# Kernel tuning notes

Hardware: AMD Instinct MI355X
Metric: run time of the kernel (lower is better)

## Reference

```python
import jax, jax.numpy as jnp
import numpy as np

N, E, B, F_IN, C, K = 200000, 3200000, 128, 128, 10, 30
D_CAT = 97  # 32+32+32+1 concatenated GCN outputs


def setup_inputs() -> dict:
    key = jax.random.key(0)
    ks = jax.random.split(key, 12)
    s = 0.1
    return {
        "x": jax.random.normal(ks[0], (N, F_IN), jnp.float32),
        "edge_index": jax.random.randint(ks[1], (2, E), 0, N, jnp.int32),
        "batch": jnp.sort(jax.random.randint(ks[2], (N,), 0, B, jnp.int32)),
        "W1": jax.random.normal(ks[3], (F_IN, 32), jnp.float32) * s,
        "b1": jnp.zeros((32,), jnp.float32),
        "W2": jax.random.normal(ks[4], (32, 32), jnp.float32) * s,
        "b2": jnp.zeros((32,), jnp.float32),
        "W3": jax.random.normal(ks[5], (32, 32), jnp.float32) * s,
        "b3": jnp.zeros((32,), jnp.float32),
        "W4": jax.random.normal(ks[6], (32, 1), jnp.float32) * s,
        "b4": jnp.zeros((1,), jnp.float32),
        "conv5_w": jax.random.normal(ks[7], (16, 1, 97), jnp.float32) * s,
        "conv5_b": jnp.zeros((16,), jnp.float32),
        "conv6_w": jax.random.normal(ks[8], (32, 16, 5), jnp.float32) * s,
        "conv6_b": jnp.zeros((32,), jnp.float32),
        "fc1_w": jax.random.normal(ks[9], (352, 128), jnp.float32) * s,
        "fc1_b": jnp.zeros((128,), jnp.float32),
        "fc2_w": jax.random.normal(ks[10], (128, C), jnp.float32) * s,
        "fc2_b": jnp.zeros((C,), jnp.float32),
    }


def _gcn(x, W, b, src, dst, enorm, self_norm):
    # PyG GCNConv: h = xW; out = sum_j norm_ij * h_j (incl. self loop) + b
    h = x @ W
    agg = jax.ops.segment_sum(h[src] * enorm[:, None], dst, num_segments=h.shape[0])
    return agg + h * self_norm[:, None] + b


def _conv1d(x, w, b, stride):
    y = jax.lax.conv_general_dilated(x, w, (stride,), 'VALID',
                                     dimension_numbers=('NCH', 'OIH', 'NCH'))
    return y + b[None, :, None]


def reference(x, edge_index, batch, W1, b1, W2, b2, W3, b3, W4, b4,
              conv5_w, conv5_b, conv6_w, conv6_b, fc1_w, fc1_b, fc2_w, fc2_b):
    src, dst = edge_index[0], edge_index[1]
    # remove_self_loops (zero edge weight) then GCN adds self loop of weight 1
    w = (src != dst).astype(x.dtype)
    deg = jax.ops.segment_sum(w, dst, num_segments=N) + 1.0
    dinv = jax.lax.rsqrt(deg)
    enorm = w * dinv[src] * dinv[dst]   # per-edge sym norm
    self_norm = 1.0 / deg               # self-loop norm = dinv[i]^2

    x1 = jnp.tanh(_gcn(x, W1, b1, src, dst, enorm, self_norm))
    x2 = jnp.tanh(_gcn(x1, W2, b2, src, dst, enorm, self_norm))
    x3 = jnp.tanh(_gcn(x2, W3, b3, src, dst, enorm, self_norm))
    x4 = jnp.tanh(_gcn(x3, W4, b4, src, dst, enorm, self_norm))
    xc = jnp.concatenate([x1, x2, x3, x4], axis=-1)  # [N, 97]

    # SortAggregation(k=30): per-graph top-k nodes by last channel (descending)
    keyf = xc[:, -1]
    graph_ids = jnp.arange(B, dtype=batch.dtype)
    scores = jnp.where(batch[None, :] == graph_ids[:, None], keyf[None, :],
                       jnp.float32(-jnp.inf))         # [B, N]
    topv, topi = jax.lax.top_k(scores, K)              # [B, K]
    feats = xc[topi]                                   # [B, K, 97]
    feats = jnp.where(jnp.isfinite(topv)[..., None], feats, 0.0)  # pad rows -> 0
    z = feats.reshape(B, 1, K * D_CAT)                 # [B, 1, 2910]

    z = jax.nn.relu(_conv1d(z, conv5_w, conv5_b, 97))  # [B, 16, 30]
    z = jax.lax.reduce_window(z, -jnp.inf, jax.lax.max,
                              (1, 1, 2), (1, 1, 2), 'VALID')  # [B, 16, 15]
    z = jax.nn.relu(_conv1d(z, conv6_w, conv6_b, 1))   # [B, 32, 11]
    z = z.reshape(B, -1)                               # [B, 352]
    h = jax.nn.relu(z @ fc1_w + fc1_b)                 # dropout = identity (eval)
    return jax.nn.log_softmax(h @ fc2_w + fc2_b, axis=-1)
```

## Files before the change

### kernel.cpp

```cpp
#include <hip/hip_runtime.h>
#include <math.h>

#define TPB 256
#define TOPK 30
#define NGRAPH 128
#define TKCAP 4096
#define BSHIFT 11
#define NBMAX 128
#define FSHIFT 8
#define NFMAX 800
#define FCAP 4608


__global__ void bhist(const int* __restrict__ src, const int* __restrict__ dst,
                      int* __restrict__ btot, int E) {
    __shared__ int bcnt[NBMAX];
    int t = threadIdx.x;
    int base = blockIdx.x * 2048;
    int lim = E - base; if (lim > 2048) lim = 2048;
    for (int i = t; i < NBMAX; i += 256) bcnt[i] = 0;
    __syncthreads();
    for (int i = t; i < lim; i += 256) {
        int s = src[base + i], d = dst[base + i];
        if (s != d) atomicAdd(&bcnt[d >> BSHIFT], 1);
    }
    __syncthreads();
    for (int i = t; i < NBMAX; i += 256)
        if (bcnt[i] > 0) atomicAdd(&btot[i], bcnt[i]);
}

__global__ void bucket_scan(const int* __restrict__ btot, int* __restrict__ bbase,
                            int nbuckets) {
    __shared__ int ls[NBMAX];
    int t = threadIdx.x;
    int v = (t < nbuckets) ? btot[t] : 0;
    ls[t] = v;
    __syncthreads();
    for (int o = 1; o < NBMAX; o <<= 1) {
        int x = 0;
        if (t >= o) x = ls[t - o];
        __syncthreads();
        ls[t] += x;
        __syncthreads();
    }
    if (t < nbuckets) bbase[t] = ls[t] - v;
}

__global__ void bin_edges(const int* __restrict__ src, const int* __restrict__ dst,
                          const int* __restrict__ bbase_g, int* __restrict__ gcur,
                          int2* __restrict__ scratch, int E) {
    __shared__ int2 eds[2048];
    __shared__ int bcnt[NBMAX], bbase[NBMAX], boff[NBMAX];
    int t = threadIdx.x;
    int base = blockIdx.x * 2048;
    int lim = E - base; if (lim > 2048) lim = 2048;
    for (int i = t; i < NBMAX; i += 256) { bcnt[i] = 0; boff[i] = 0; }
    __syncthreads();
    for (int i = t; i < lim; i += 256) {
        int s = src[base + i], d = dst[base + i];
        if (s == d) d = -1;
        eds[i] = make_int2(s, d);
        if (d >= 0) atomicAdd(&bcnt[d >> BSHIFT], 1);
    }
    __syncthreads();
    for (int i = t; i < NBMAX; i += 256) {
        if (bcnt[i] > 0)
            bbase[i] = bbase_g[i] + atomicAdd(&gcur[i], bcnt[i]);
    }
    __syncthreads();
    for (int i = t; i < lim; i += 256) {
        int2 ed = eds[i];
        if (ed.y >= 0) {
            int b = ed.y >> BSHIFT;
            int pos = bbase[b] + atomicAdd(&boff[b], 1);
            scratch[pos] = ed;
        }
    }
}

__global__ void bucket_count(const int2* __restrict__ scratch,
                             const int* __restrict__ bbase, const int* __restrict__ btot,
                             int* __restrict__ cnt, float* __restrict__ dinv,
                             float* __restrict__ snorm, int N) {
    __shared__ int hist[1 << BSHIFT];
    int b = blockIdx.x, t = threadIdx.x;
    int nlo = b << BSHIFT;
    int nn = N - nlo; if (nn > (1 << BSHIFT)) nn = 1 << BSHIFT;
    for (int i = t; i < (1 << BSHIFT); i += 256) hist[i] = 0;
    __syncthreads();
    int lo = bbase[b], hi = lo + btot[b];
    for (int e = lo + t; e < hi; e += 256)
        atomicAdd(&hist[scratch[e].y - nlo], 1);
    __syncthreads();
    for (int i = t; i < nn; i += 256) {
        int c = hist[i];
        cnt[nlo + i] = c;
        float deg = (float)c + 1.0f;
        dinv[nlo + i] = 1.0f / sqrtf(deg);
        snorm[nlo + i] = 1.0f / deg;
    }
}

__global__ void scan1(const int* __restrict__ cnt, int* __restrict__ outp,
                      int* __restrict__ bsum, int n) {
    __shared__ int ls[256];
    int t = threadIdx.x;
    int base = blockIdx.x * 1024;
    int v[4], ex[4];
    int run = 0;
    #pragma unroll
    for (int j = 0; j < 4; ++j) {
        int i = base + t * 4 + j;
        v[j] = (i < n) ? cnt[i] : 0;
        ex[j] = run;
        run += v[j];
    }
    ls[t] = run;
    __syncthreads();
    for (int o2 = 1; o2 < 256; o2 <<= 1) {
        int xv = 0;
        if (t >= o2) xv = ls[t - o2];
        __syncthreads();
        ls[t] += xv;
        __syncthreads();
    }
    int tbase = ls[t] - run;
    #pragma unroll
    for (int j = 0; j < 4; ++j) {
        int i = base + t * 4 + j;
        if (i < n) outp[i] = tbase + ex[j];
    }
    if (t == 255) bsum[blockIdx.x] = ls[255];
}

__global__ void scan2(int* __restrict__ bsum, int nb) {
    __shared__ int ls[256];
    int t = threadIdx.x;
    int v = (t < nb) ? bsum[t] : 0;
    ls[t] = v;
    __syncthreads();
    for (int o2 = 1; o2 < 256; o2 <<= 1) {
        int xv = 0;
        if (t >= o2) xv = ls[t - o2];
        __syncthreads();
        ls[t] += xv;
        __syncthreads();
    }
    if (t < nb) bsum[t] = ls[t] - v;
    if (t == 255) bsum[nb] = ls[255];
}

__global__ void scan3(int* __restrict__ rowptr, const int* __restrict__ bsum, int n, int nb) {
    int i = blockIdx.x * blockDim.x + threadIdx.x;
    if (i < n) rowptr[i] += bsum[i >> 10];
    if (i == 0) rowptr[n] = bsum[nb];
}

__global__ void bin2(const int2* __restrict__ scratch, const int* __restrict__ rowptr,
                     int* __restrict__ fcur, int2* __restrict__ scratch2, int N, int E) {
    __shared__ int fcnt[NFMAX], fbase[NFMAX], foff[NFMAX];
    int t = threadIdx.x;
    int En = rowptr[N];
    int base = blockIdx.x * 8192;
    if (base >= En) return;
    int lim = En - base; if (lim > 8192) lim = 8192;
    for (int i = t; i < NFMAX; i += 256) { fcnt[i] = 0; foff[i] = 0; }
    __syncthreads();
    for (int i = t; i < lim; i += 256) {
        int d = scratch[base + i].y;
        atomicAdd(&fcnt[d >> FSHIFT], 1);
    }
    __syncthreads();
    for (int fi = t; fi < NFMAX; fi += 256) {
        if (fcnt[fi] > 0)
            fbase[fi] = rowptr[fi << FSHIFT] + atomicAdd(&fcur[fi], fcnt[fi]);
    }
    __syncthreads();
    for (int i = t; i < lim; i += 256) {
        int2 ed = scratch[base + i];
        int fi = ed.y >> FSHIFT;
        int pos = fbase[fi] + atomicAdd(&foff[fi], 1);
        scratch2[pos] = ed;
    }
}

__global__ __launch_bounds__(256) void scatter_sort(const int2* __restrict__ scratch2,
                                                    const int* __restrict__ rowptr,
                                                    const float* __restrict__ dinv,
                                                    int2* __restrict__ eprec, int N) {
    __shared__ int srcA[FCAP], dstA[FCAP], inv[FCAP];
    __shared__ int hist[1 << FSHIFT];
    __shared__ int hcur[1 << FSHIFT];
    int f = blockIdx.x, t = threadIdx.x;
    int nlo = f << FSHIFT;
    int nhi = nlo + (1 << FSHIFT); if (nhi > N) nhi = N;
    int lo = rowptr[nlo], hi = rowptr[nhi];
    int span = hi - lo;
    for (int i = t; i < (1 << FSHIFT); i += 256) hist[i] = 0;
    __syncthreads();
    if (span <= FCAP) {
        for (int i = t; i < span; i += 256) {
            int2 ed = scratch2[lo + i];
            srcA[i] = ed.x; dstA[i] = ed.y;
            atomicAdd(&hist[ed.y - nlo], 1);
        }
        __syncthreads();
        int v = hist[t];
        hcur[t] = v;
        __syncthreads();
        for (int o = 1; o < 256; o <<= 1) {
            int x = (t >= o) ? hcur[t - o] : 0;
            __syncthreads();
            hcur[t] += x;
            __syncthreads();
        }
        int excl = hcur[t] - v;
        __syncthreads();
        hcur[t] = excl;
        __syncthreads();
        for (int i = t; i < span; i += 256) {
            int slot = atomicAdd(&hcur[dstA[i] - nlo], 1);
            inv[slot] = i;
        }
        __syncthreads();
        for (int p = t; p < span; p += 256) {
            int i = inv[p];
            int s = srcA[i], d = dstA[i];
            eprec[lo + p] = make_int2(s, __float_as_int(dinv[s] * dinv[d]));
        }
    } else {
        for (int e = lo + t; e < hi; e += 256) {
            int2 ed = scratch2[e];
            int d = ed.y;
            int p = rowptr[d] + atomicAdd(&hist[d - nlo], 1);
            eprec[p] = make_int2(ed.x, __float_as_int(dinv[ed.x] * dinv[d]));
        }
    }
}


__global__ void mm_128_32(const float* __restrict__ X, const float* __restrict__ W,
                          float* __restrict__ H, int n) {
    __shared__ float Ws[128 * 32];
    __shared__ float xs[32 * 128];
    int t = threadIdx.x;
    int rbase = blockIdx.x * 32;
    #pragma unroll
    for (int j = 0; j < 4; ++j) {
        int idx = t + 256 * j;
        *(float4*)(Ws + idx * 4) = *(const float4*)(W + idx * 4);
        int row = rbase + (idx >> 5);
        float4 v = make_float4(0.f, 0.f, 0.f, 0.f);
        if (row < n) v = *(const float4*)(X + (long)rbase * 128 + idx * 4);
        *(float4*)(xs + idx * 4) = v;
    }
    __syncthreads();
    int c4 = (t & 7) * 4, r = t >> 3;
    int row = rbase + r;
    if (row >= n) return;
    float ac0 = 0.f, ac1 = 0.f, ac2 = 0.f, ac3 = 0.f;
    #pragma unroll 8
    for (int k0 = 0; k0 < 128; k0 += 4) {
        float4 xv = *(const float4*)(xs + r * 128 + k0);
        #pragma unroll
        for (int j = 0; j < 4; ++j) {
            float xj = (j == 0) ? xv.x : (j == 1) ? xv.y : (j == 2) ? xv.z : xv.w;
            float4 wv = *(const float4*)(Ws + (k0 + j) * 32 + c4);
            ac0 += xj * wv.x; ac1 += xj * wv.y; ac2 += xj * wv.z; ac3 += xj * wv.w;
        }
    }
    *(float4*)(H + (long)row * 32 + c4) = make_float4(ac0, ac1, ac2, ac3);
}

__global__ void mm_32_32(const float* __restrict__ X, const float* __restrict__ W,
                         float* __restrict__ H, int n) {
    __shared__ float Ws[32 * 32];
    __shared__ float xs[32 * 32];
    int t = threadIdx.x;
    int rbase = blockIdx.x * 32;
    {
        *(float4*)(Ws + t * 4) = *(const float4*)(W + t * 4);
        int row = rbase + (t >> 3);
        float4 v = make_float4(0.f, 0.f, 0.f, 0.f);
        if (row < n) v = *(const float4*)(X + (long)rbase * 32 + t * 4);
        *(float4*)(xs + t * 4) = v;
    }
    __syncthreads();
    int c4 = (t & 7) * 4, r = t >> 3;
    int row = rbase + r;
    if (row >= n) return;
    float ac0 = 0.f, ac1 = 0.f, ac2 = 0.f, ac3 = 0.f;
    #pragma unroll
    for (int k0 = 0; k0 < 32; k0 += 4) {
        float4 xv = *(const float4*)(xs + r * 32 + k0);
        #pragma unroll
        for (int j = 0; j < 4; ++j) {
            float xj = (j == 0) ? xv.x : (j == 1) ? xv.y : (j == 2) ? xv.z : xv.w;
            float4 wv = *(const float4*)(Ws + (k0 + j) * 32 + c4);
            ac0 += xj * wv.x; ac1 += xj * wv.y; ac2 += xj * wv.z; ac3 += xj * wv.w;
        }
    }
    *(float4*)(H + (long)row * 32 + c4) = make_float4(ac0, ac1, ac2, ac3);
}

__global__ void mm_32_1(const float* __restrict__ X, const float* __restrict__ W,
                        float* __restrict__ H4, int n) {
    int gid = blockIdx.x * blockDim.x + threadIdx.x;
    int node = gid >> 3, l = gid & 7;
    if (node >= n) return;
    float4 v = *(const float4*)(X + (long)node * 32 + l * 4);
    float s = v.x * W[l * 4] + v.y * W[l * 4 + 1] + v.z * W[l * 4 + 2] + v.w * W[l * 4 + 3];
    s += __shfl_xor(s, 1, 64);
    s += __shfl_xor(s, 2, 64);
    s += __shfl_xor(s, 4, 64);
    if (l == 0) H4[node] = s;
}


__global__ void agg32(const float* __restrict__ H, const int2* __restrict__ eprec,
                      const int* __restrict__ rowptr,
                      const float* __restrict__ snorm, const float* __restrict__ bias,
                      float* __restrict__ OUT, int n) {
    int gid = blockIdx.x * blockDim.x + threadIdx.x;
    int node = gid >> 3, l = gid & 7;
    if (node >= n) return;
    int beg = rowptr[node], end = rowptr[node + 1];
    float ax = 0.f, ay = 0.f, az = 0.f, aw = 0.f;
    int e0 = beg;
    for (; e0 + 8 <= end; e0 += 8) {
        int2 ed = eprec[e0 + l];
        int ss[8]; float ww[8];
        #pragma unroll
        for (int j = 0; j < 8; ++j) {
            ss[j] = __shfl(ed.x, j, 8);
            ww[j] = __shfl(__int_as_float(ed.y), j, 8);
        }
        float4 hv[8];
        #pragma unroll
        for (int j = 0; j < 8; ++j)
            hv[j] = *(const float4*)(H + (long)ss[j] * 32 + l * 4);
        #pragma unroll
        for (int j = 0; j < 8; ++j) {
            ax += hv[j].x * ww[j]; ay += hv[j].y * ww[j];
            az += hv[j].z * ww[j]; aw += hv[j].w * ww[j];
        }
    }
    if (e0 < end) {
        int m = end - e0;
        int2 ed = (l < m) ? eprec[e0 + l] : make_int2(0, 0);
        for (int j = 0; j < m; ++j) {
            int s = __shfl(ed.x, j, 8);
            float w = __shfl(__int_as_float(ed.y), j, 8);
            float4 hv = *(const float4*)(H + (long)s * 32 + l * 4);
            ax += hv.x * w; ay += hv.y * w; az += hv.z * w; aw += hv.w * w;
        }
    }
    float sn = snorm[node];
    float4 hv = *(const float4*)(H + (long)node * 32 + l * 4);
    float4 bv = *(const float4*)(bias + l * 4);
    float4 o;
    o.x = tanhf(ax + hv.x * sn + bv.x);
    o.y = tanhf(ay + hv.y * sn + bv.y);
    o.z = tanhf(az + hv.z * sn + bv.z);
    o.w = tanhf(aw + hv.w * sn + bv.w);
    *(float4*)(OUT + (long)node * 32 + l * 4) = o;
}

__global__ void agg1(const float* __restrict__ H4, const int2* __restrict__ eprec,
                     const int* __restrict__ rowptr,
                     const float* __restrict__ snorm, const float* __restrict__ b4,
                     float* __restrict__ X4, int n) {
    int node = blockIdx.x * blockDim.x + threadIdx.x;
    if (node >= n) return;
    int beg = rowptr[node], end = rowptr[node + 1];
    float acc = 0.f;
    for (int e = beg; e < end; ++e) {
        int2 ed = eprec[e];
        acc += H4[ed.x] * __int_as_float(ed.y);
    }
    X4[node] = tanhf(acc + H4[node] * snorm[node] + b4[0]);
}


__global__ void graph_start(const int* __restrict__ batch, int* __restrict__ gstart,
                            int n, int B) {
    int i = blockIdx.x * blockDim.x + threadIdx.x;
    if (i >= n) return;
    int b = batch[i];
    int bp = (i == 0) ? -1 : batch[i - 1];
    for (int g = bp + 1; g <= b; ++g) gstart[g] = i;
    if (i == n - 1) {
        for (int g = b + 1; g <= B; ++g) gstart[g] = n;
    }
}

__global__ __launch_bounds__(64) void topk_kernel(const float* __restrict__ keyf,
                                                  const int* __restrict__ gstart,
                                                  int* __restrict__ topi) {
    int g = blockIdx.x;
    int t = threadIdx.x;
    __shared__ float vals[TKCAP];
    __shared__ int selg[TOPK];
    int beg = gstart[g], end = gstart[g + 1];
    int range = end - beg;

    if (range <= 2048) {
        float rv[32];
        #pragma unroll
        for (int j = 0; j < 32; ++j) {
            int i = t + (j << 6);
            rv[j] = (i < range) ? keyf[beg + i] : -INFINITY;
        }
        for (int k = 0; k < TOPK; ++k) {
            float best = -INFINITY;
            int bj = -1;
            #pragma unroll
            for (int j = 0; j < 32; ++j)
                if (rv[j] > best) { best = rv[j]; bj = j; }
            int bi = (bj < 0) ? 0x7fffffff : (bj << 6) + t;
            #pragma unroll
            for (int off = 1; off < 64; off <<= 1) {
                float ov = __shfl_xor(best, off, 64);
                int oi = __shfl_xor(bi, off, 64);
                if (ov > best || (ov == best && oi < bi)) { best = ov; bi = oi; }
            }
            if (t == 0)
                topi[g * TOPK + k] = (bi == 0x7fffffff) ? -1 : beg + bi;
            if (bi != 0x7fffffff && (bi & 63) == t) {
                int wj = bi >> 6;
                #pragma unroll
                for (int j = 0; j < 32; ++j)
                    if (j == wj) rv[j] = -INFINITY;
            }
        }
        return;
    }

    int lim = range < TKCAP ? range : TKCAP;
    for (int i = t; i < lim; i += 64) vals[i] = keyf[beg + i];
    __syncthreads();
    for (int k = 0; k < TOPK; ++k) {
        float best = -INFINITY;
        int bi = 0x7fffffff;
        for (int i = t; i < lim; i += 64) {
            float v = vals[i];
            if (v > best) { best = v; bi = i; }
        }
        for (int i = TKCAP + t; i < range; i += 64) {
            int gi = beg + i;
            bool taken = false;
            for (int j = 0; j < k; ++j)
                if (selg[j] == gi) { taken = true; break; }
            if (taken) continue;
            float v = keyf[gi];
            if (v > best || (v == best && i < bi)) { best = v; bi = i; }
        }
        #pragma unroll
        for (int off = 1; off < 64; off <<= 1) {
            float ov = __shfl_xor(best, off, 64);
            int oi = __shfl_xor(bi, off, 64);
            if (ov > best || (ov == best && oi < bi)) { best = ov; bi = oi; }
        }
        if (t == 0) {
            int gl = (bi == 0x7fffffff) ? -1 : beg + bi;
            selg[k] = gl;
            topi[g * TOPK + k] = gl;
            if (bi != 0x7fffffff && bi < TKCAP) vals[bi] = -INFINITY;
        }
        __syncthreads();
    }
}


__global__ void head_kernel(const float* __restrict__ x1, const float* __restrict__ x2,
                            const float* __restrict__ x3, const float* __restrict__ x4,
                            const int* __restrict__ topi,
                            const float* __restrict__ w5, const float* __restrict__ b5,
                            const float* __restrict__ w6, const float* __restrict__ b6,
                            const float* __restrict__ fw1, const float* __restrict__ fb1,
                            const float* __restrict__ fw2, const float* __restrict__ fb2,
                            float* __restrict__ out) {
    int b = blockIdx.x;
    int t = threadIdx.x;
    __shared__ float feats[TOPK][97];
    __shared__ float c5[16][30];
    __shared__ float p6[16][15];
    __shared__ float z[352];
    __shared__ float hh[128];
    __shared__ float oo[10];

    for (int idx = t; idx < TOPK * 97; idx += 256) {
        int k = idx / 97, j = idx % 97;
        int node = topi[b * TOPK + k];
        float v = 0.f;
        if (node >= 0) {
            if (j < 32) v = x1[(long)node * 32 + j];
            else if (j < 64) v = x2[(long)node * 32 + (j - 32)];
            else if (j < 96) v = x3[(long)node * 32 + (j - 64)];
            else v = x4[node];
        }
        feats[k][j] = v;
    }
    __syncthreads();

    for (int idx = t; idx < 16 * 30; idx += 256) {
        int oc = idx / 30, k = idx % 30;
        float acc = b5[oc];
        for (int j = 0; j < 97; ++j) acc += w5[oc * 97 + j] * feats[k][j];
        c5[oc][k] = fmaxf(acc, 0.f);
    }
    __syncthreads();

    for (int idx = t; idx < 16 * 15; idx += 256) {
        int oc = idx / 15, k = idx % 15;
        p6[oc][k] = fmaxf(c5[oc][2 * k], c5[oc][2 * k + 1]);
    }
    __syncthreads();

    for (int idx = t; idx < 32 * 11; idx += 256) {
        int oc = idx / 11, tt = idx % 11;
        float acc = b6[oc];
        for (int ic = 0; ic < 16; ++ic)
            for (int j = 0; j < 5; ++j)
                acc += w6[(oc * 16 + ic) * 5 + j] * p6[ic][tt + j];
        z[idx] = fmaxf(acc, 0.f);
    }
    __syncthreads();

    if (t < 128) {
        float acc = fb1[t];
        for (int i = 0; i < 352; ++i) acc += z[i] * fw1[i * 128 + t];
        hh[t] = fmaxf(acc, 0.f);
    }
    __syncthreads();

    if (t < 10) {
        float acc = fb2[t];
        for (int j = 0; j < 128; ++j) acc += hh[j] * fw2[j * 10 + t];
        oo[t] = acc;
    }
    __syncthreads();

    if (t < 10) {
        float m = -INFINITY;
        for (int c = 0; c < 10; ++c) m = fmaxf(m, oo[c]);
        float s = 0.f;
        for (int c = 0; c < 10; ++c) s += expf(oo[c] - m);
        out[b * 10 + t] = oo[t] - m - logf(s);
    }
}


extern "C" void kernel_launch(void* const* d_in, const int* in_sizes, int n_in,
                              void* d_out, int out_size, void* d_ws, size_t ws_size,
                              hipStream_t stream) {
    const float* x     = (const float*)d_in[0];
    const int*   ei    = (const int*)d_in[1];
    const int*   batch = (const int*)d_in[2];
    const float* W1 = (const float*)d_in[3];
    const float* b1 = (const float*)d_in[4];
    const float* W2 = (const float*)d_in[5];
    const float* b2 = (const float*)d_in[6];
    const float* W3 = (const float*)d_in[7];
    const float* b3 = (const float*)d_in[8];
    const float* W4 = (const float*)d_in[9];
    const float* b4 = (const float*)d_in[10];
    const float* w5 = (const float*)d_in[11];
    const float* b5 = (const float*)d_in[12];
    const float* w6 = (const float*)d_in[13];
    const float* b6 = (const float*)d_in[14];
    const float* fw1 = (const float*)d_in[15];
    const float* fb1 = (const float*)d_in[16];
    const float* fw2 = (const float*)d_in[17];
    const float* fb2 = (const float*)d_in[18];

    const int N = in_sizes[0] / 128;
    const int E = in_sizes[1] / 2;
    const int* src = ei;
    const int* dst = ei + E;

    char* w = (char*)d_ws;
    size_t off = 0;
    auto alloc = [&](size_t bytes) -> void* {
        void* p = w + off;
        off = (off + bytes + 255) & ~(size_t)255;
        return p;
    };

    int*   cnt    = (int*)alloc((size_t)N * 4);
    int*   rowptr = (int*)alloc((size_t)(N + 1) * 4);
    int*   bsum   = (int*)alloc(4096 * 4);
    int*   gcur   = (int*)alloc(NBMAX * 4);
    int*   btot   = (int*)alloc(NBMAX * 4);
    int*   bbase  = (int*)alloc(NBMAX * 4);
    int*   fcur   = (int*)alloc(NFMAX * 4);
    float* dinv   = (float*)alloc((size_t)N * 4);
    float* snorm  = (float*)alloc((size_t)N * 4);
    int2*  eprec  = (int2*)alloc((size_t)E * 8);
    float* hbuf   = (float*)alloc((size_t)N * 32 * 4);
    float* x1     = (float*)alloc((size_t)N * 32 * 4);
    float* x2     = (float*)alloc((size_t)N * 32 * 4);
    float* x3     = (float*)alloc((size_t)N * 32 * 4);
    float* h4     = (float*)alloc((size_t)N * 4);
    float* x4     = (float*)alloc((size_t)N * 4);
    int*   gstart = (int*)alloc((size_t)(NGRAPH + 1) * 4);
    int*   topi   = (int*)alloc((size_t)NGRAPH * TOPK * 4);

    int2* scratch  = (int2*)hbuf;
    int2* scratch2 = (int2*)x1;

    hipMemsetAsync(gcur, 0, NBMAX * 4, stream);
    hipMemsetAsync(btot, 0, NBMAX * 4, stream);
    hipMemsetAsync(fcur, 0, NFMAX * 4, stream);

    const int NB = (N + (1 << BSHIFT) - 1) >> BSHIFT;
    const int NF = (N + (1 << FSHIFT) - 1) >> FSHIFT;
    const int EB = (E + 2047) / 2048;

    bhist<<<EB, TPB, 0, stream>>>(src, dst, btot, E);
    bucket_scan<<<1, NBMAX, 0, stream>>>(btot, bbase, NB);
    bin_edges<<<EB, TPB, 0, stream>>>(src, dst, bbase, gcur, scratch, E);
    bucket_count<<<NB, TPB, 0, stream>>>(scratch, bbase, btot, cnt, dinv, snorm, N);

    int nb = (N + 1023) / 1024;
    scan1<<<nb, 256, 0, stream>>>(cnt, rowptr, bsum, N);
    scan2<<<1, 256, 0, stream>>>(bsum, nb);
    scan3<<<(N + TPB - 1) / TPB, TPB, 0, stream>>>(rowptr, bsum, N, nb);

    bin2<<<(E + 8191) / 8192, TPB, 0, stream>>>(scratch, rowptr, fcur, scratch2, N, E);
    scatter_sort<<<NF, 256, 0, stream>>>(scratch2, rowptr, dinv, eprec, N);

    mm_128_32<<<(N + 31) / 32, 256, 0, stream>>>(x, W1, hbuf, N);
    agg32<<<((size_t)N * 8 + TPB - 1) / TPB, TPB, 0, stream>>>(hbuf, eprec, rowptr,
                                                               snorm, b1, x1, N);
    mm_32_32<<<(N + 31) / 32, 256, 0, stream>>>(x1, W2, hbuf, N);
    agg32<<<((size_t)N * 8 + TPB - 1) / TPB, TPB, 0, stream>>>(hbuf, eprec, rowptr,
                                                               snorm, b2, x2, N);
    mm_32_32<<<(N + 31) / 32, 256, 0, stream>>>(x2, W3, hbuf, N);
    agg32<<<((size_t)N * 8 + TPB - 1) / TPB, TPB, 0, stream>>>(hbuf, eprec, rowptr,
                                                               snorm, b3, x3, N);
    mm_32_1<<<((size_t)N * 8 + TPB - 1) / TPB, TPB, 0, stream>>>(x3, W4, h4, N);
    agg1<<<(N + TPB - 1) / TPB, TPB, 0, stream>>>(h4, eprec, rowptr, snorm, b4, x4, N);

    graph_start<<<(N + TPB - 1) / TPB, TPB, 0, stream>>>(batch, gstart, N, NGRAPH);
    topk_kernel<<<NGRAPH, 64, 0, stream>>>(x4, gstart, topi);
    head_kernel<<<NGRAPH, 256, 0, stream>>>(x1, x2, x3, x4, topi, w5, b5, w6, b6,
                                            fw1, fb1, fw2, fb2, (float*)d_out);
}
```

Before: 563.0 us.

## Fold CSR scan into bucket_count, drop bin2 pass, fuse top-k with head

Each coarse bucket now computes its own per-node exclusive scan offset from the bucket base, which replaces the three global scan kernels. The second binning pass goes away: each fine block scans its whole coarse bucket and keeps only edges whose destination falls in its range. Graph boundaries are found by binary search over batch, and top-k selection is fused into the head kernel. This cuts kernel launches and one full edge copy, at the cost of each coarse bucket being read eight times in scatter_sort.

```diff
diff --git a/kernel.cpp b/kernel.cpp
--- a/kernel.cpp
+++ b/kernel.cpp
@@ -8,7 +8,6 @@
 #define BSHIFT 11
 #define NBMAX 128
 #define FSHIFT 8
-#define NFMAX 800
 #define FCAP 4608
 
 
@@ -80,9 +79,10 @@
 
 __global__ void bucket_count(const int2* __restrict__ scratch,
                              const int* __restrict__ bbase, const int* __restrict__ btot,
-                             int* __restrict__ cnt, float* __restrict__ dinv,
-                             float* __restrict__ snorm, int N) {
+                             int* __restrict__ rowptr, float* __restrict__ dinv,
+                             float* __restrict__ snorm, int N, int NB) {
     __shared__ int hist[1 << BSHIFT];
+    __shared__ int ls2[256];
     int b = blockIdx.x, t = threadIdx.x;
     int nlo = b << BSHIFT;
     int nn = N - nlo; if (nn > (1 << BSHIFT)) nn = 1 << BSHIFT;
@@ -92,117 +92,60 @@
     for (int e = lo + t; e < hi; e += 256)
         atomicAdd(&hist[scratch[e].y - nlo], 1);
     __syncthreads();
-    for (int i = t; i < nn; i += 256) {
-        int c = hist[i];
-        cnt[nlo + i] = c;
-        float deg = (float)c + 1.0f;
-        dinv[nlo + i] = 1.0f / sqrtf(deg);
-        snorm[nlo + i] = 1.0f / deg;
-    }
-}
-
-__global__ void scan1(const int* __restrict__ cnt, int* __restrict__ outp,
-                      int* __restrict__ bsum, int n) {
-    __shared__ int ls[256];
-    int t = threadIdx.x;
-    int base = blockIdx.x * 1024;
-    int v[4], ex[4];
-    int run = 0;
+    int loc[8]; int run = 0;
     #pragma unroll
-    for (int j = 0; j < 4; ++j) {
-        int i = base + t * 4 + j;
-        v[j] = (i < n) ? cnt[i] : 0;
-        ex[j] = run;
-        run += v[j];
-    }
-    ls[t] = run;
-    __syncthreads();
-    for (int o2 = 1; o2 < 256; o2 <<= 1) {
-        int xv = 0;
-        if (t >= o2) xv = ls[t - o2];
-        __syncthreads();
-        ls[t] += xv;
-        __syncthreads();
-    }
-    int tbase = ls[t] - run;
+    for (int j = 0; j < 8; ++j) { loc[j] = run; run += hist[t * 8 + j]; }
+    ls2[t] = run;
+    __syncthreads();
+    for (int o = 1; o < 256; o <<= 1) {
+        int x = (t >= o) ? ls2[t - o] : 0;
+        __syncthreads();
+        ls2[t] += x;
+        __syncthreads();
+    }
+    int base = bbase[b] + ls2[t] - run;
     #pragma unroll
-    for (int j = 0; j < 4; ++j) {
-        int i = base + t * 4 + j;
-        if (i < n) outp[i] = tbase + ex[j];
-    }
-    if (t == 255) bsum[blockIdx.x] = ls[255];
-}
-
-__global__ void scan2(int* __restrict__ bsum, int nb) {
-    __shared__ int ls[256];
-    int t = threadIdx.x;
-    int v = (t < nb) ? bsum[t] : 0;
-    ls[t] = v;
-    __syncthreads();
-    for (int o2 = 1; o2 < 256; o2 <<= 1) {
-        int xv = 0;
-        if (t >= o2) xv = ls[t - o2];
-        __syncthreads();
-        ls[t] += xv;
-        __syncthreads();
-    }
-    if (t < nb) bsum[t] = ls[t] - v;
-    if (t == 255) bsum[nb] = ls[255];
-}
-
-__global__ void scan3(int* __restrict__ rowptr, const int* __restrict__ bsum, int n, int nb) {
-    int i = blockIdx.x * blockDim.x + threadIdx.x;
-    if (i < n) rowptr[i] += bsum[i >> 10];
-    if (i == 0) rowptr[n] = bsum[nb];
-}
-
-__global__ void bin2(const int2* __restrict__ scratch, const int* __restrict__ rowptr,
-                     int* __restrict__ fcur, int2* __restrict__ scratch2, int N, int E) {
-    __shared__ int fcnt[NFMAX], fbase[NFMAX], foff[NFMAX];
-    int t = threadIdx.x;
-    int En = rowptr[N];
-    int base = blockIdx.x * 8192;
-    if (base >= En) return;
-    int lim = En - base; if (lim > 8192) lim = 8192;
-    for (int i = t; i < NFMAX; i += 256) { fcnt[i] = 0; foff[i] = 0; }
-    __syncthreads();
-    for (int i = t; i < lim; i += 256) {
-        int d = scratch[base + i].y;
-        atomicAdd(&fcnt[d >> FSHIFT], 1);
-    }
-    __syncthreads();
-    for (int fi = t; fi < NFMAX; fi += 256) {
-        if (fcnt[fi] > 0)
-            fbase[fi] = rowptr[fi << FSHIFT] + atomicAdd(&fcur[fi], fcnt[fi]);
-    }
-    __syncthreads();
-    for (int i = t; i < lim; i += 256) {
-        int2 ed = scratch[base + i];
-        int fi = ed.y >> FSHIFT;
-        int pos = fbase[fi] + atomicAdd(&foff[fi], 1);
-        scratch2[pos] = ed;
-    }
-}
-
-__global__ __launch_bounds__(256) void scatter_sort(const int2* __restrict__ scratch2,
+    for (int j = 0; j < 8; ++j) {
+        int i = t * 8 + j;
+        if (i < nn) {
+            rowptr[nlo + i] = base + loc[j];
+            int c = hist[i];
+            float deg = (float)c + 1.0f;
+            dinv[nlo + i] = 1.0f / sqrtf(deg);
+            snorm[nlo + i] = 1.0f / deg;
+        }
+    }
+    if (b == NB - 1 && t == 0) rowptr[N] = bbase[b] + btot[b];
+}
+
+__global__ __launch_bounds__(256) void scatter_sort(const int2* __restrict__ scratch,
+                                                    const int* __restrict__ bbase,
+                                                    const int* __restrict__ btot,
                                                     const int* __restrict__ rowptr,
                                                     const float* __restrict__ dinv,
                                                     int2* __restrict__ eprec, int N) {
     __shared__ int srcA[FCAP], dstA[FCAP], inv[FCAP];
     __shared__ int hist[1 << FSHIFT];
     __shared__ int hcur[1 << FSHIFT];
+    __shared__ int kcnt;
     int f = blockIdx.x, t = threadIdx.x;
     int nlo = f << FSHIFT;
     int nhi = nlo + (1 << FSHIFT); if (nhi > N) nhi = N;
     int lo = rowptr[nlo], hi = rowptr[nhi];
     int span = hi - lo;
+    int cb = f >> (BSHIFT - FSHIFT);
+    int clo = bbase[cb], chi = clo + btot[cb];
     for (int i = t; i < (1 << FSHIFT); i += 256) hist[i] = 0;
+    if (t == 0) kcnt = 0;
     __syncthreads();
     if (span <= FCAP) {
-        for (int i = t; i < span; i += 256) {
-            int2 ed = scratch2[lo + i];
-            srcA[i] = ed.x; dstA[i] = ed.y;
-            atomicAdd(&hist[ed.y - nlo], 1);
+        for (int e = clo + t; e < chi; e += 256) {
+            int2 ed = scratch[e];
+            if ((ed.y >> FSHIFT) == f) {
+                int p = atomicAdd(&kcnt, 1);
+                srcA[p] = ed.x; dstA[p] = ed.y;
+                atomicAdd(&hist[ed.y - nlo], 1);
+            }
         }
         __syncthreads();
         int v = hist[t];
@@ -229,11 +172,13 @@
             eprec[lo + p] = make_int2(s, __float_as_int(dinv[s] * dinv[d]));
         }
     } else {
-        for (int e = lo + t; e < hi; e += 256) {
-            int2 ed = scratch2[e];
-            int d = ed.y;
-            int p = rowptr[d] + atomicAdd(&hist[d - nlo], 1);
-            eprec[p] = make_int2(ed.x, __float_as_int(dinv[ed.x] * dinv[d]));
+        for (int e = clo + t; e < chi; e += 256) {
+            int2 ed = scratch[e];
+            if ((ed.y >> FSHIFT) == f) {
+                int d = ed.y;
+                int p = rowptr[d] + atomicAdd(&hist[d - nlo], 1);
+                eprec[p] = make_int2(ed.x, __float_as_int(dinv[ed.x] * dinv[d]));
+            }
         }
     }
 }
@@ -382,106 +327,23 @@
 }
 
 
-__global__ void graph_start(const int* __restrict__ batch, int* __restrict__ gstart,
-                            int n, int B) {
-    int i = blockIdx.x * blockDim.x + threadIdx.x;
-    if (i >= n) return;
-    int b = batch[i];
-    int bp = (i == 0) ? -1 : batch[i - 1];
-    for (int g = bp + 1; g <= b; ++g) gstart[g] = i;
-    if (i == n - 1) {
-        for (int g = b + 1; g <= B; ++g) gstart[g] = n;
-    }
-}
-
-__global__ __launch_bounds__(64) void topk_kernel(const float* __restrict__ keyf,
-                                                  const int* __restrict__ gstart,
-                                                  int* __restrict__ topi) {
+__global__ __launch_bounds__(256) void topk_head(
+        const float* __restrict__ x1, const float* __restrict__ x2,
+        const float* __restrict__ x3, const float* __restrict__ x4,
+        const int* __restrict__ batch, int Nn,
+        const float* __restrict__ w5, const float* __restrict__ b5,
+        const float* __restrict__ w6, const float* __restrict__ b6,
+        const float* __restrict__ fw1, const float* __restrict__ fb1,
+        const float* __restrict__ fw2, const float* __restrict__ fb2,
+        float* __restrict__ out) {
     int g = blockIdx.x;
     int t = threadIdx.x;
+    __shared__ int topi_l[TOPK];
+    __shared__ int selg[TOPK];
+    __shared__ int begend[2];
     __shared__ float vals[TKCAP];
-    __shared__ int selg[TOPK];
-    int beg = gstart[g], end = gstart[g + 1];
-    int range = end - beg;
-
-    if (range <= 2048) {
-        float rv[32];
-        #pragma unroll
-        for (int j = 0; j < 32; ++j) {
-            int i = t + (j << 6);
-            rv[j] = (i < range) ? keyf[beg + i] : -INFINITY;
-        }
-        for (int k = 0; k < TOPK; ++k) {
-            float best = -INFINITY;
-            int bj = -1;
-            #pragma unroll
-            for (int j = 0; j < 32; ++j)
-                if (rv[j] > best) { best = rv[j]; bj = j; }
-            int bi = (bj < 0) ? 0x7fffffff : (bj << 6) + t;
-            #pragma unroll
-            for (int off = 1; off < 64; off <<= 1) {
-                float ov = __shfl_xor(best, off, 64);
-                int oi = __shfl_xor(bi, off, 64);
-                if (ov > best || (ov == best && oi < bi)) { best = ov; bi = oi; }
-            }
-            if (t == 0)
-                topi[g * TOPK + k] = (bi == 0x7fffffff) ? -1 : beg + bi;
-            if (bi != 0x7fffffff && (bi & 63) == t) {
-                int wj = bi >> 6;
-                #pragma unroll
-                for (int j = 0; j < 32; ++j)
-                    if (j == wj) rv[j] = -INFINITY;
-            }
-        }
-        return;
-    }
-
-    int lim = range < TKCAP ? range : TKCAP;
-    for (int i = t; i < lim; i += 64) vals[i] = keyf[beg + i];
-    __syncthreads();
-    for (int k = 0; k < TOPK; ++k) {
-        float best = -INFINITY;
-        int bi = 0x7fffffff;
-        for (int i = t; i < lim; i += 64) {
-            float v = vals[i];
-            if (v > best) { best = v; bi = i; }
-        }
-        for (int i = TKCAP + t; i < range; i += 64) {
-            int gi = beg + i;
-            bool taken = false;
-            for (int j = 0; j < k; ++j)
-                if (selg[j] == gi) { taken = true; break; }
-            if (taken) continue;
-            float v = keyf[gi];
-            if (v > best || (v == best && i < bi)) { best = v; bi = i; }
-        }
-        #pragma unroll
-        for (int off = 1; off < 64; off <<= 1) {
-            float ov = __shfl_xor(best, off, 64);
-            int oi = __shfl_xor(bi, off, 64);
-            if (ov > best || (ov == best && oi < bi)) { best = ov; bi = oi; }
-        }
-        if (t == 0) {
-            int gl = (bi == 0x7fffffff) ? -1 : beg + bi;
-            selg[k] = gl;
-            topi[g * TOPK + k] = gl;
-            if (bi != 0x7fffffff && bi < TKCAP) vals[bi] = -INFINITY;
-        }
-        __syncthreads();
-    }
-}
-
-
-__global__ void head_kernel(const float* __restrict__ x1, const float* __restrict__ x2,
-                            const float* __restrict__ x3, const float* __restrict__ x4,
-                            const int* __restrict__ topi,
-                            const float* __restrict__ w5, const float* __restrict__ b5,
-                            const float* __restrict__ w6, const float* __restrict__ b6,
-                            const float* __restrict__ fw1, const float* __restrict__ fb1,
-                            const float* __restrict__ fw2, const float* __restrict__ fb2,
-                            float* __restrict__ out) {
-    int b = blockIdx.x;
-    int t = threadIdx.x;
+    __shared__ float wbv[4];
+    __shared__ int wbi[4];
     __shared__ float feats[TOPK][97];
     __shared__ float c5[16][30];
     __shared__ float p6[16][15];
@@ -489,9 +351,95 @@
     __shared__ float hh[128];
     __shared__ float oo[10];
 
+    if (t == 0) {
+        int lo = 0, hi = Nn;
+        while (lo < hi) { int m = (lo + hi) >> 1; if (batch[m] < g) lo = m + 1; else hi = m; }
+        begend[0] = lo;
+        lo = 0; hi = Nn;
+        while (lo < hi) { int m = (lo + hi) >> 1; if (batch[m] < g + 1) lo = m + 1; else hi = m; }
+        begend[1] = lo;
+    }
+    __syncthreads();
+    int beg = begend[0], end = begend[1];
+    int range = end - beg;
+
+    if (range <= 2048) {
+        if (t < 64) {
+            float rv[32];
+            #pragma unroll
+            for (int j = 0; j < 32; ++j) {
+                int i = t + (j << 6);
+                rv[j] = (i < range) ? x4[beg + i] : -INFINITY;
+            }
+            for (int k = 0; k < TOPK; ++k) {
+                float best = -INFINITY;
+                int bj = -1;
+                #pragma unroll
+                for (int j = 0; j < 32; ++j)
+                    if (rv[j] > best) { best = rv[j]; bj = j; }
+                int bi = (bj < 0) ? 0x7fffffff : (bj << 6) + t;
+                #pragma unroll
+                for (int off = 1; off < 64; off <<= 1) {
+                    float ov = __shfl_xor(best, off, 64);
+                    int oi = __shfl_xor(bi, off, 64);
+                    if (ov > best || (ov == best && oi < bi)) { best = ov; bi = oi; }
+                }
+                if (t == 0)
+                    topi_l[k] = (bi == 0x7fffffff) ? -1 : beg + bi;
+                if (bi != 0x7fffffff && (bi & 63) == t) {
+                    int wj = bi >> 6;
+                    #pragma unroll
+                    for (int j = 0; j < 32; ++j)
+                        if (j == wj) rv[j] = -INFINITY;
+                }
+            }
+        }
+    } else {
+        int lim = range < TKCAP ? range : TKCAP;
+        for (int i = t; i < lim; i += 256) vals[i] = x4[beg + i];
+        __syncthreads();
+        for (int k = 0; k < TOPK; ++k) {
+            float best = -INFINITY;
+            int bi = 0x7fffffff;
+            for (int i = t; i < lim; i += 256) {
+                float v = vals[i];
+                if (v > best) { best = v; bi = i; }
+            }
+            for (int i = TKCAP + t; i < range; i += 256) {
+                int gi = beg + i;
+                bool taken = false;
+                for (int j = 0; j < k; ++j)
+                    if (selg[j] == gi) { taken = true; break; }
+                if (taken) continue;
+                float v = vals[0];
+                v = x4[gi];
+                if (v > best || (v == best && i < bi)) { best = v; bi = i; }
+            }
+            #pragma unroll
+            for (int off = 1; off < 64; off <<= 1) {
+                float ov = __shfl_xor(best, off, 64);
+                int oi = __shfl_xor(bi, off, 64);
+                if (ov > best || (ov == best && oi < bi)) { best = ov; bi = oi; }
+            }
+            if ((t & 63) == 0) { wbv[t >> 6] = best; wbi[t >> 6] = bi; }
+            __syncthreads();
+            if (t == 0) {
+                float bv = wbv[0]; int bi0 = wbi[0];
+                for (int wv = 1; wv < 4; ++wv)
+                    if (wbv[wv] > bv || (wbv[wv] == bv && wbi[wv] < bi0)) { bv = wbv[wv]; bi0 = wbi[wv]; }
+                int gl = (bi0 == 0x7fffffff) ? -1 : beg + bi0;
+                selg[k] = gl;
+                topi_l[k] = gl;
+                if (bi0 != 0x7fffffff && bi0 < TKCAP) vals[bi0] = -INFINITY;
+            }
+            __syncthreads();
+        }
+    }
+    __syncthreads();
+
     for (int idx = t; idx < TOPK * 97; idx += 256) {
         int k = idx / 97, j = idx % 97;
-        int node = topi[b * TOPK + k];
+        int node = topi_l[k];
         float v = 0.f;
         if (node >= 0) {
             if (j < 32) v = x1[(long)node * 32 + j];
@@ -546,7 +494,7 @@
         for (int c = 0; c < 10; ++c) m = fmaxf(m, oo[c]);
         float s = 0.f;
         for (int c = 0; c < 10; ++c) s += expf(oo[c] - m);
-        out[b * 10 + t] = oo[t] - m - logf(s);
+        out[g * 10 + t] = oo[t] - m - logf(s);
     }
 }
 
@@ -587,13 +535,10 @@
         return p;
     };
 
-    int*   cnt    = (int*)alloc((size_t)N * 4);
-    int*   rowptr = (int*)alloc((size_t)(N + 1) * 4);
-    int*   bsum   = (int*)alloc(4096 * 4);
     int*   gcur   = (int*)alloc(NBMAX * 4);
     int*   btot   = (int*)alloc(NBMAX * 4);
     int*   bbase  = (int*)alloc(NBMAX * 4);
-    int*   fcur   = (int*)alloc(NFMAX * 4);
+    int*   rowptr = (int*)alloc((size_t)(N + 1) * 4);
     float* dinv   = (float*)alloc((size_t)N * 4);
     float* snorm  = (float*)alloc((size_t)N * 4);
     int2*  eprec  = (int2*)alloc((size_t)E * 8);
@@ -603,15 +548,10 @@
     float* x3     = (float*)alloc((size_t)N * 32 * 4);
     float* h4     = (float*)alloc((size_t)N * 4);
     float* x4     = (float*)alloc((size_t)N * 4);
-    int*   gstart = (int*)alloc((size_t)(NGRAPH + 1) * 4);
-    int*   topi   = (int*)alloc((size_t)NGRAPH * TOPK * 4);
-
-    int2* scratch  = (int2*)hbuf;
-    int2* scratch2 = (int2*)x1;
-
-    hipMemsetAsync(gcur, 0, NBMAX * 4, stream);
-    hipMemsetAsync(btot, 0, NBMAX * 4, stream);
-    hipMemsetAsync(fcur, 0, NFMAX * 4, stream);
+
+    int2* scratch = (int2*)hbuf;
+
+    hipMemsetAsync(gcur, 0, 2 * NBMAX * 4, stream);
 
     const int NB = (N + (1 << BSHIFT) - 1) >> BSHIFT;
     const int NF = (N + (1 << FSHIFT) - 1) >> FSHIFT;
@@ -620,15 +560,8 @@
     bhist<<<EB, TPB, 0, stream>>>(src, dst, btot, E);
     bucket_scan<<<1, NBMAX, 0, stream>>>(btot, bbase, NB);
     bin_edges<<<EB, TPB, 0, stream>>>(src, dst, bbase, gcur, scratch, E);
-    bucket_count<<<NB, TPB, 0, stream>>>(scratch, bbase, btot, cnt, dinv, snorm, N);
-
-    int nb = (N + 1023) / 1024;
-    scan1<<<nb, 256, 0, stream>>>(cnt, rowptr, bsum, N);
-    scan2<<<1, 256, 0, stream>>>(bsum, nb);
-    scan3<<<(N + TPB - 1) / TPB, TPB, 0, stream>>>(rowptr, bsum, N, nb);
-
-    bin2<<<(E + 8191) / 8192, TPB, 0, stream>>>(scratch, rowptr, fcur, scratch2, N, E);
-    scatter_sort<<<NF, 256, 0, stream>>>(scratch2, rowptr, dinv, eprec, N);
+    bucket_count<<<NB, TPB, 0, stream>>>(scratch, bbase, btot, rowptr, dinv, snorm, N, NB);
+    scatter_sort<<<NF, 256, 0, stream>>>(scratch, bbase, btot, rowptr, dinv, eprec, N);
 
     mm_128_32<<<(N + 31) / 32, 256, 0, stream>>>(x, W1, hbuf, N);
     agg32<<<((size_t)N * 8 + TPB - 1) / TPB, TPB, 0, stream>>>(hbuf, eprec, rowptr,
@@ -642,8 +575,7 @@
     mm_32_1<<<((size_t)N * 8 + TPB - 1) / TPB, TPB, 0, stream>>>(x3, W4, h4, N);
     agg1<<<(N + TPB - 1) / TPB, TPB, 0, stream>>>(h4, eprec, rowptr, snorm, b4, x4, N);
 
-    graph_start<<<(N + TPB - 1) / TPB, TPB, 0, stream>>>(batch, gstart, N, NGRAPH);
-    topk_kernel<<<NGRAPH, 64, 0, stream>>>(x4, gstart, topi);
-    head_kernel<<<NGRAPH, 256, 0, stream>>>(x1, x2, x3, x4, topi, w5, b5, w6, b6,
-                                            fw1, fb1, fw2, fb2, (float*)d_out);
-}
+    topk_head<<<NGRAPH, 256, 0, stream>>>(x1, x2, x3, x4, batch, N,
+                                          w5, b5, w6, b6, fw1, fb1, fw2, fb2,
+                                          (float*)d_out);
+}
```

After: 638.8 us. +13.4%, slower.
